# Kernel tuning notes

Hardware: AMD Instinct MI355X
Metric: run time of the kernel (lower is better)

## Reference

```python
import jax, jax.numpy as jnp
import numpy as np

B = 8          # batch size (static)
GRID = 1024    # spatial grid H = W
PER = 25000    # active sites per batch item
N = B * PER

_OFFSETS = [(dx, dy) for dx in (-1, 0, 1) for dy in (-1, 0, 1)]  # 3x3 kernel


def _build_sparse_inputs():
    """Sample unique active 2D coords per batch item and build the 3x3
    submanifold neighbor map: nbr[i, k] = index of neighbor site at kernel
    offset k, or -1 if that coordinate is inactive."""
    rng = np.random.default_rng(0)
    bs, xs, ys = [], [], []
    for b in range(B):
        flat = rng.choice(GRID * GRID, size=PER, replace=False)
        bs.append(np.full(PER, b, np.int64))
        xs.append((flat // GRID).astype(np.int64))
        ys.append((flat % GRID).astype(np.int64))
    bb = np.concatenate(bs); xx = np.concatenate(xs); yy = np.concatenate(ys)
    # hash lookup table: (b, x, y) -> site index
    lut = np.full(B * GRID * GRID, -1, np.int64)
    lut[bb * GRID * GRID + xx * GRID + yy] = np.arange(N, dtype=np.int64)
    nbr = np.full((N, 9), -1, np.int64)
    for k, (dx, dy) in enumerate(_OFFSETS):
        nx, ny = xx + dx, yy + dy
        ok = (nx >= 0) & (nx < GRID) & (ny >= 0) & (ny < GRID)
        key = bb * GRID * GRID + np.clip(nx, 0, GRID - 1) * GRID + np.clip(ny, 0, GRID - 1)
        nbr[:, k] = np.where(ok, lut[key], -1)
    return bb, nbr


def setup_inputs() -> dict:
    key = jax.random.key(0)
    k1, k2, k3 = jax.random.split(key, 3)
    batch_np, nbr_np = _build_sparse_inputs()
    feats = jax.random.normal(k1, (N, 3), dtype=jnp.float32)
    # He (kaiming normal, relu): std = sqrt(2 / fan_in), fan_in = 9 * Cin
    W1 = jax.random.normal(k2, (9, 3, 256), dtype=jnp.float32) * np.sqrt(2.0 / (9 * 3))
    W2 = jax.random.normal(k3, (9, 256, 256), dtype=jnp.float32) * np.sqrt(2.0 / (9 * 256))
    return {
        "feats": feats,
        "W1": W1,
        "W2": W2,
        "nbr": jnp.asarray(nbr_np),
        "batch_ids": jnp.asarray(batch_np),
    }


def _subm_conv(feat, W, nbr):
    """Submanifold 3x3 conv: out[i] = sum_k feat[nbr[i,k]] @ W[k] over valid
    neighbors. feat: [N, Cin], W: [9, Cin, Cout], nbr: [N, 9] -> [N, Cout]."""
    out = jnp.zeros((feat.shape[0], W.shape[2]), dtype=feat.dtype)
    for k in range(9):  # fixed small kernel loop
        idx = nbr[:, k]
        valid = (idx >= 0).astype(feat.dtype)[:, None]
        g = feat[jnp.maximum(idx, 0)] * valid  # masked gather [N, Cin]
        out = out + g @ W[k]
    return out


def reference(feats, W1, W2, nbr, batch_ids):
    h = jax.nn.relu(_subm_conv(feats, W1, nbr))   # [N, 256]
    h = jax.nn.relu(_subm_conv(h, W2, nbr))       # [N, 256]
    # global average pool per batch item -> [B, 256]
    sums = jax.ops.segment_sum(h, batch_ids, num_segments=B)
    counts = jax.ops.segment_sum(jnp.ones((h.shape[0],), h.dtype), batch_ids, num_segments=B)
    return sums / counts[:, None]
```

## Files before the change

### kernel.cpp

```cpp
#include <hip/hip_runtime.h>
#include <hip/hip_bf16.h>

typedef __attribute__((ext_vector_type(8))) short bh8;
typedef __attribute__((ext_vector_type(4))) float f32x4;

#define NB 8
#define SLOTS 64
#define CAP 6144
#define CROWS 36864
#define CBLOCKS 256
#define FROWS 64

__device__ __forceinline__ void gld_lds16(const void* g, void* l) {
  __builtin_amdgcn_global_load_lds(
      (const __attribute__((address_space(1))) void*)g,
      (__attribute__((address_space(3))) void*)l, 16, 0, 0);
}

__device__ __forceinline__ unsigned short f2bu(float f) {
  union { __hip_bfloat16 h; unsigned short u; } cv;
  cv.h = __float2bfloat16(f);
  return cv.u;
}
__device__ __forceinline__ float bu2f(unsigned short u) {
  return __uint_as_float(((unsigned)u) << 16);
}

__global__ void w1t_kernel(const float* __restrict__ W1, short* __restrict__ w1bt) {
  const int n = threadIdx.x;
#pragma unroll
  for (int kk = 0; kk < 32; ++kk)
    w1bt[n * 32 + kk] = (kk < 27) ? (short)f2bu(W1[kk * 256 + n]) : (short)0;
}

__device__ __forceinline__ float3 ldf3(const float* __restrict__ f,
                                       const int* s_nbr, int idx) {
  int s = s_nbr[idx];
  long long sc = (s < 0) ? 0 : s;
  float3 r;
  r.x = f[3 * sc]; r.y = f[3 * sc + 1]; r.z = f[3 * sc + 2];
  if (s < 0) { r.x = 0.f; r.y = 0.f; r.z = 0.f; }
  return r;
}

__global__ __launch_bounds__(256, 2) void conv1_mfma_kernel(
    const float* __restrict__ feats, const short* __restrict__ w1bt,
    const int* __restrict__ nbr, __hip_bfloat16* __restrict__ h1b, int N) {
  __shared__ int s_nbr[64 * 9];
  const int tid = threadIdx.x;
  const int base = blockIdx.x * 64;

  for (int t = tid; t < 64 * 9; t += 256) s_nbr[t] = nbr[base * 9 + t];
  __syncthreads();

  const int wave = tid >> 6, lane = tid & 63;
  const int q = lane >> 4, m16 = lane & 15;
  const int rbase = (wave * 16 + m16) * 9;

  bh8 a;
  if (q == 0) {
    float3 t0 = ldf3(feats, s_nbr, rbase + 0);
    float3 t1 = ldf3(feats, s_nbr, rbase + 1);
    float3 t2 = ldf3(feats, s_nbr, rbase + 2);
    a[0] = (short)f2bu(t0.x); a[1] = (short)f2bu(t0.y); a[2] = (short)f2bu(t0.z);
    a[3] = (short)f2bu(t1.x); a[4] = (short)f2bu(t1.y); a[5] = (short)f2bu(t1.z);
    a[6] = (short)f2bu(t2.x); a[7] = (short)f2bu(t2.y);
  } else if (q == 1) {
    float3 t2 = ldf3(feats, s_nbr, rbase + 2);
    float3 t3 = ldf3(feats, s_nbr, rbase + 3);
    float3 t4 = ldf3(feats, s_nbr, rbase + 4);
    float3 t5 = ldf3(feats, s_nbr, rbase + 5);
    a[0] = (short)f2bu(t2.z);
    a[1] = (short)f2bu(t3.x); a[2] = (short)f2bu(t3.y); a[3] = (short)f2bu(t3.z);
    a[4] = (short)f2bu(t4.x); a[5] = (short)f2bu(t4.y); a[6] = (short)f2bu(t4.z);
    a[7] = (short)f2bu(t5.x);
  } else if (q == 2) {
    float3 t5 = ldf3(feats, s_nbr, rbase + 5);
    float3 t6 = ldf3(feats, s_nbr, rbase + 6);
    float3 t7 = ldf3(feats, s_nbr, rbase + 7);
    a[0] = (short)f2bu(t5.y); a[1] = (short)f2bu(t5.z);
    a[2] = (short)f2bu(t6.x); a[3] = (short)f2bu(t6.y); a[4] = (short)f2bu(t6.z);
    a[5] = (short)f2bu(t7.x); a[6] = (short)f2bu(t7.y); a[7] = (short)f2bu(t7.z);
  } else {
    float3 t8 = ldf3(feats, s_nbr, rbase + 8);
    a[0] = (short)f2bu(t8.x); a[1] = (short)f2bu(t8.y); a[2] = (short)f2bu(t8.z);
    a[3] = 0; a[4] = 0; a[5] = 0; a[6] = 0; a[7] = 0;
  }

  f32x4 acc[16];
#pragma unroll
  for (int nj = 0; nj < 16; ++nj) {
    bh8 b = *(const bh8*)(w1bt + (nj * 16 + m16) * 32 + q * 8);
    acc[nj] = __builtin_amdgcn_mfma_f32_16x16x32_bf16(a, b, (f32x4)0.f, 0, 0, 0);
  }

  const int growb = base + wave * 16 + q * 4;
#pragma unroll
  for (int rr = 0; rr < 4; ++rr) {
    __hip_bfloat16* rowp = h1b + (long long)(growb + rr) * 256 + m16;
#pragma unroll
    for (int nj = 0; nj < 16; ++nj)
      rowp[nj * 16] = __float2bfloat16(fmaxf(acc[nj][rr], 0.f));
  }
}

__global__ __launch_bounds__(256) void w2t_kernel(
    const float* __restrict__ W2, __hip_bfloat16* __restrict__ w2bt) {
  __shared__ float tile[16][256];
  int k = blockIdx.x >> 4, t = blockIdx.x & 15;
  int tid = threadIdx.x;
#pragma unroll
  for (int r = 0; r < 16; ++r) tile[r][tid] = W2[k * 65536 + (t * 16 + r) * 256 + tid];
  __syncthreads();
#pragma unroll
  for (int r = 0; r < 16; ++r)
    w2bt[k * 65536 + tid * 256 + t * 16 + r] = __float2bfloat16(tile[r][tid]);
}

__global__ __launch_bounds__(256) void build_pairs_kernel(
    const int* __restrict__ nbr, const int* __restrict__ bid,
    int* __restrict__ nOff, int* __restrict__ cnt, float* __restrict__ bcnt,
    int* __restrict__ cidmap, int* __restrict__ crow,
    int* __restrict__ psrc, int* __restrict__ pcnt_cid,
    int* __restrict__ pairlist, int N) {
  __shared__ int l_cnt[10];
  __shared__ int l_base[10];
  __shared__ int l_bcnt[NB];
  const int tid = threadIdx.x;
  if (tid < 10) l_cnt[tid] = 0;
  if (tid < NB) l_bcnt[tid] = 0;
  __syncthreads();

  const int i = blockIdx.x * 256 + tid;
  const bool active = (i < N);
  int s[9];
  int kpos[9];
  int loc_cid = -1;
  if (active) {
#pragma unroll
    for (int k = 0; k < 9; ++k) s[k] = nbr[i * 9 + k];
    bool any = false;
#pragma unroll
    for (int k = 0; k < 9; ++k)
      if (k != 4 && s[k] >= 0) any = true;
    if (any) {
      loc_cid = atomicAdd(&l_cnt[9], 1);
#pragma unroll
      for (int k = 0; k < 9; ++k) {
        kpos[k] = -1;
        if (k != 4 && s[k] >= 0) kpos[k] = atomicAdd(&l_cnt[k], 1);
      }
    }
    atomicAdd(&l_bcnt[bid[i]], 1);
  }
  __syncthreads();

  if (tid < 9) l_base[tid] = (l_cnt[tid] > 0) ? atomicAdd(&cnt[tid], l_cnt[tid]) : 0;
  else if (tid == 9) l_base[9] = (l_cnt[9] > 0) ? atomicAdd(nOff, l_cnt[9]) : 0;
  if (tid >= 32 && tid < 32 + NB && l_bcnt[tid - 32] > 0)
    atomicAdd(&bcnt[tid - 32], (float)l_bcnt[tid - 32]);
  __syncthreads();

  if (active) {
    int cid = -1;
    if (loc_cid >= 0) {
      cid = l_base[9] + loc_cid;
      if (cid >= CROWS) cid = -1;
    }
    cidmap[i] = cid;
    if (cid >= 0) {
      crow[cid] = i;
#pragma unroll
      for (int k = 0; k < 9; ++k) {
        if (k == 4 || kpos[k] < 0 || s[k] < 0) continue;
        int pos = l_base[k] + kpos[k];
        if (pos < CAP) {
          psrc[k * CAP + pos] = s[k];
          int slot = atomicAdd(&pcnt_cid[cid], 1);
          if (slot < 8) pairlist[cid * 8 + slot] = k * CAP + pos;
        }
      }
    }
  }
}

__global__ __launch_bounds__(256, 2) void ctap_kernel(
    const __hip_bfloat16* __restrict__ h1, const __hip_bfloat16* __restrict__ w2bt,
    const int* __restrict__ nOffp, const int* __restrict__ crow,
    unsigned short* __restrict__ h2cb) {
  int nc = *nOffp;
  if (nc > CROWS) nc = CROWS;
  const int base = blockIdx.x * 64;
  if (base >= nc) return;

  __shared__ int s_src[64];
  const int tid = threadIdx.x;
  if (tid < 64) {
    int m = base + tid;
    s_src[tid] = (m < nc) ? crow[m] : 0;
  }

  const int wave = tid >> 6, lane = tid & 63, q = lane >> 4, m16 = lane & 15;
  const short* h1s = (const short*)h1;
  const short* wts = (const short*)w2bt + 4 * 65536;

  bh8 breg[4][8];
#pragma unroll
  for (int nj = 0; nj < 4; ++nj)
#pragma unroll
    for (int ko = 0; ko < 8; ++ko)
      breg[nj][ko] = *(const bh8*)(wts + (wave * 64 + nj * 16 + m16) * 256 + ko * 32 + q * 8);
  __syncthreads();

  bh8 aA[8];
  {
    const short* ap = h1s + (long long)s_src[m16] * 256 + q * 8;
#pragma unroll
    for (int ko = 0; ko < 8; ++ko) aA[ko] = *(const bh8*)(ap + ko * 32);
  }

#pragma unroll
  for (int t = 0; t < 4; ++t) {
    bh8 aN[8];
    if (t < 3) {
      const short* ap = h1s + (long long)s_src[(t + 1) * 16 + m16] * 256 + q * 8;
#pragma unroll
      for (int ko = 0; ko < 8; ++ko) aN[ko] = *(const bh8*)(ap + ko * 32);
    }
    f32x4 acc[4];
#pragma unroll
    for (int ko = 0; ko < 8; ++ko)
#pragma unroll
      for (int nj = 0; nj < 4; ++nj)
        acc[nj] = __builtin_amdgcn_mfma_f32_16x16x32_bf16(
            aA[ko], breg[nj][ko], (ko == 0) ? (f32x4)0.f : acc[nj], 0, 0, 0);
#pragma unroll
    for (int r = 0; r < 4; ++r) {
      int m = base + t * 16 + q * 4 + r;
      if (m >= nc) continue;
#pragma unroll
      for (int nj = 0; nj < 4; ++nj)
        h2cb[(long long)m * 256 + wave * 64 + nj * 16 + m16] = f2bu(acc[nj][r]);
    }
#pragma unroll
    for (int ko = 0; ko < 8; ++ko) aA[ko] = aN[ko];
    if (base + (t + 1) * 16 >= nc) break;
  }
}

__global__ __launch_bounds__(256, 2) void off_gemm_kernel(
    const __hip_bfloat16* __restrict__ h1, const __hip_bfloat16* __restrict__ w2bt,
    const int* __restrict__ cnt, const int* __restrict__ psrc,
    unsigned short* __restrict__ pout) {
  const int bpk = CAP / 64;
  int koff = blockIdx.x / bpk;
  int grp = blockIdx.x - koff * bpk;
  int k = koff + (koff >= 4 ? 1 : 0);
  int cntk = cnt[k];
  const int base = grp * 64;
  if (base >= cntk) return;

  __shared__ int s_src[64];
  const int tid = threadIdx.x;
  if (tid < 64) {
    int m = base + tid;
    s_src[tid] = (m < cntk) ? psrc[k * CAP + m] : 0;
  }

  const int wave = tid >> 6, lane = tid & 63, q = lane >> 4, m16 = lane & 15;
  const short* h1s = (const short*)h1;
  const short* wts = (const short*)w2bt + k * 65536;

  bh8 breg[4][8];
#pragma unroll
  for (int nj = 0; nj < 4; ++nj)
#pragma unroll
    for (int ko = 0; ko < 8; ++ko)
      breg[nj][ko] = *(const bh8*)(wts + (wave * 64 + nj * 16 + m16) * 256 + ko * 32 + q * 8);
  __syncthreads();

  bh8 aA[8];
  {
    const short* ap = h1s + (long long)s_src[m16] * 256 + q * 8;
#pragma unroll
    for (int ko = 0; ko < 8; ++ko) aA[ko] = *(const bh8*)(ap + ko * 32);
  }

#pragma unroll
  for (int t = 0; t < 4; ++t) {
    bh8 aN[8];
    if (t < 3) {
      const short* ap = h1s + (long long)s_src[(t + 1) * 16 + m16] * 256 + q * 8;
#pragma unroll
      for (int ko = 0; ko < 8; ++ko) aN[ko] = *(const bh8*)(ap + ko * 32);
    }
    f32x4 acc[4];
#pragma unroll
    for (int ko = 0; ko < 8; ++ko)
#pragma unroll
      for (int nj = 0; nj < 4; ++nj)
        acc[nj] = __builtin_amdgcn_mfma_f32_16x16x32_bf16(
            aA[ko], breg[nj][ko], (ko == 0) ? (f32x4)0.f : acc[nj], 0, 0, 0);
#pragma unroll
    for (int r = 0; r < 4; ++r) {
      int m = base + t * 16 + q * 4 + r;
      if (m >= cntk) continue;
      const long long rowb = (long long)(k * CAP + m) * 256;
#pragma unroll
      for (int nj = 0; nj < 4; ++nj)
        pout[rowb + wave * 64 + nj * 16 + m16] = f2bu(acc[nj][r]);
    }
#pragma unroll
    for (int ko = 0; ko < 8; ++ko) aA[ko] = aN[ko];
    if (base + (t + 1) * 16 >= cntk) break;
  }
}

__global__ __launch_bounds__(512, 2) void center_gemm_kernel(
    const __hip_bfloat16* __restrict__ h1, const __hip_bfloat16* __restrict__ w2bt,
    const int* __restrict__ cidmap, const int* __restrict__ bid,
    float* __restrict__ psums, int N) {
  __shared__ __align__(16) short Abuf[2][64 * 256];

  const int tid = threadIdx.x;
  const int wave = tid >> 6, lane = tid & 63;
  const int q = lane >> 4, m16 = lane & 15;
  const int wc = wave << 5;
  const int slot = blockIdx.x & (SLOTS - 1);

  const short* h1s = (const short*)h1;
  const short* wts = (const short*)w2bt + 4 * 65536;

  bh8 breg[2][8];
#pragma unroll
  for (int nj = 0; nj < 2; ++nj)
#pragma unroll
    for (int ko = 0; ko < 8; ++ko)
      breg[nj][ko] = *(const bh8*)(wts + (wc + nj * 16 + m16) * 256 + ko * 32 + q * 8);

  const int nchunk = (N + 63) >> 6;
  const int span = (nchunk + CBLOCKS - 1) / CBLOCKS;
  const int c0 = blockIdx.x * span;
  if (c0 >= nchunk) return;
  int c1 = c0 + span;
  if (c1 > nchunk) c1 = nchunk;

  const int lrow = lane >> 5;
  const int jch  = lane & 31;

#define STAGE_CHUNK(cc, b)                                                     \
  {                                                                            \
    _Pragma("unroll") for (int t = 0; t < 4; ++t) {                            \
      int lr = (wave << 3) + (t << 1) + lrow;                                  \
      int g = ((cc) << 6) + lr;                                                \
      if (g >= N) g = N - 1;                                                   \
      int js = jch ^ (lr & 31);                                                \
      const short* src = h1s + (long long)g * 256 + (js << 3);                 \
      short* dst = &Abuf[b][((wave << 3) + (t << 1)) << 8];                    \
      gld_lds16((const void*)src, (void*)dst);                                 \
    }                                                                          \
  }

#define FLUSH_SACC()                                                           \
  if (cur_b0 >= 0) {                                                           \
    _Pragma("unroll") for (int lb = 0; lb < 2; ++lb) {                         \
      _Pragma("unroll") for (int nj = 0; nj < 2; ++nj) {                       \
        float v = sacc[lb][nj];                                                \
        v += __shfl_xor(v, 16, 64);                                            \
        v += __shfl_xor(v, 32, 64);                                            \
        if (q == 0 && v != 0.f) {                                              \
          int b = cur_b0 + lb;                                                 \
          if (b < NB)                                                          \
            atomicAdd(&psums[(slot * NB + b) * 256 + wc + nj * 16 + m16], v);  \
        }                                                                      \
      }                                                                        \
    }                                                                          \
  }

  STAGE_CHUNK(c0, 0);
  int cur = 0;
  int cur_b0 = -1;
  float sacc[2][2];
#pragma unroll
  for (int lb = 0; lb < 2; ++lb)
#pragma unroll
    for (int nj = 0; nj < 2; ++nj) sacc[lb][nj] = 0.f;

  for (int c = c0; c < c1; ++c) {
    __syncthreads();

    int4 bid4[4], cid4[4];
#pragma unroll
    for (int mi = 0; mi < 4; ++mi) {
      const int rb = (c << 6) + mi * 16 + q * 4;
      bid4[mi] = *(const int4*)(&bid[rb]);
      cid4[mi] = *(const int4*)(&cidmap[rb]);
    }
    const int b0 = bid[c << 6];

    if (c + 1 < c1) STAGE_CHUNK(c + 1, cur ^ 1);

    const short* Ab = &Abuf[cur][0];
    const short* abase[4];
    int xr[4];
#pragma unroll
    for (int mi = 0; mi < 4; ++mi) {
      int R = mi * 16 + m16;
      xr[mi] = R & 31;
      abase[mi] = Ab + (R << 8);
    }

    f32x4 acc[4][2];
#pragma unroll
    for (int ko = 0; ko < 8; ++ko) {
      bh8 a[4];
#pragma unroll
      for (int mi = 0; mi < 4; ++mi)
        a[mi] = *(const bh8*)(abase[mi] + (((ko * 4 + q) ^ xr[mi]) << 3));
#pragma unroll
      for (int mi = 0; mi < 4; ++mi)
#pragma unroll
        for (int nj = 0; nj < 2; ++nj)
          acc[mi][nj] = __builtin_amdgcn_mfma_f32_16x16x32_bf16(
              a[mi], breg[nj][ko], (ko == 0) ? (f32x4)0.f : acc[mi][nj], 0, 0, 0);
    }

    if (b0 != cur_b0) {
      FLUSH_SACC();
#pragma unroll
      for (int lb = 0; lb < 2; ++lb)
#pragma unroll
        for (int nj = 0; nj < 2; ++nj) sacc[lb][nj] = 0.f;
      cur_b0 = b0;
    }
#pragma unroll
    for (int mi = 0; mi < 4; ++mi) {
      const int bb[4] = {bid4[mi].x, bid4[mi].y, bid4[mi].z, bid4[mi].w};
      const int cc4[4] = {cid4[mi].x, cid4[mi].y, cid4[mi].z, cid4[mi].w};
      const int rb = (c << 6) + mi * 16 + q * 4;
#pragma unroll
      for (int rr = 0; rr < 4; ++rr) {
        if (rb + rr >= N) continue;
        if (cc4[rr] >= 0) continue;
        const int lb = (bb[rr] != b0) ? 1 : 0;
#pragma unroll
        for (int nj = 0; nj < 2; ++nj)
          sacc[lb][nj] += fmaxf(acc[mi][nj][rr], 0.f);
      }
    }

    cur ^= 1;
  }
  FLUSH_SACC();
#undef STAGE_CHUNK
#undef FLUSH_SACC
}

__global__ __launch_bounds__(256) void fixup_kernel(
    const unsigned short* __restrict__ h2cb, const unsigned short* __restrict__ pout,
    const int* __restrict__ pairlist, const int* __restrict__ pcnt_cid,
    const int* __restrict__ crow, const int* __restrict__ bid,
    const int* __restrict__ nOffp, float* __restrict__ psums) {
  __shared__ float lsum[NB * 256];
  __shared__ int s_b[FROWS], s_np[FROWS], s_pl[FROWS * 8];
  int nc = *nOffp;
  if (nc > CROWS) nc = CROWS;
  const int t0 = blockIdx.x * FROWS;
  if (t0 >= nc) return;
  const int tid = threadIdx.x;

  if (tid < FROWS) {
    int m = t0 + tid;
    bool v = (m < nc);
    s_b[tid] = v ? bid[crow[m]] : -1;
    int np = v ? pcnt_cid[m] : 0;
    s_np[tid] = (np > 8) ? 8 : np;
  }
  for (int i = tid; i < FROWS * 8; i += 256) {
    int m = t0 + (i >> 3);
    s_pl[i] = (m < nc) ? pairlist[m * 8 + (i & 7)] : 0;
  }
#pragma unroll
  for (int b = 0; b < NB; ++b) lsum[b * 256 + tid] = 0.f;
  __syncthreads();

  const int g = tid >> 6;
  const int cg = tid & 63;
  const ushort4* h2v = (const ushort4*)h2cb;
  const ushort4* pov = (const ushort4*)pout;

  float4 s0 = {0.f, 0.f, 0.f, 0.f}, s1 = {0.f, 0.f, 0.f, 0.f};
  const int r0 = g * 16;
  const int b0 = s_b[r0];
  int b1 = -1;
  for (int r = r0; r < r0 + 16; ++r) {
    const int b = s_b[r];
    if (b < 0) break;
    ushort4 u = h2v[(long long)(t0 + r) * 64 + cg];
    float4 x = {bu2f(u.x), bu2f(u.y), bu2f(u.z), bu2f(u.w)};
    const int np = s_np[r];
    for (int j = 0; j < np; ++j) {
      ushort4 p = pov[(long long)s_pl[r * 8 + j] * 64 + cg];
      x.x += bu2f(p.x); x.y += bu2f(p.y); x.z += bu2f(p.z); x.w += bu2f(p.w);
    }
    x.x = fmaxf(x.x, 0.f); x.y = fmaxf(x.y, 0.f);
    x.z = fmaxf(x.z, 0.f); x.w = fmaxf(x.w, 0.f);
    if (b == b0) {
      s0.x += x.x; s0.y += x.y; s0.z += x.z; s0.w += x.w;
    } else {
      b1 = b;
      s1.x += x.x; s1.y += x.y; s1.z += x.z; s1.w += x.w;
    }
  }
  if (b0 >= 0) {
    float* p0 = &lsum[b0 * 256 + cg * 4];
    atomicAdd(p0 + 0, s0.x); atomicAdd(p0 + 1, s0.y);
    atomicAdd(p0 + 2, s0.z); atomicAdd(p0 + 3, s0.w);
  }
  if (b1 >= 0 && b1 < NB) {
    float* p1 = &lsum[b1 * 256 + cg * 4];
    atomicAdd(p1 + 0, s1.x); atomicAdd(p1 + 1, s1.y);
    atomicAdd(p1 + 2, s1.z); atomicAdd(p1 + 3, s1.w);
  }
  __syncthreads();

  const int slot = blockIdx.x & (SLOTS - 1);
#pragma unroll
  for (int b = 0; b < NB; ++b) {
    float v = lsum[b * 256 + tid];
    if (v != 0.f) atomicAdd(&psums[(slot * NB + b) * 256 + tid], v);
  }
}

__global__ void finalize_kernel(const float* __restrict__ psums,
                                const float* __restrict__ bcnt,
                                float* __restrict__ out) {
  int b = blockIdx.x, c = threadIdx.x;
  float s = 0.f;
  for (int t = 0; t < SLOTS; ++t) s += psums[(t * NB + b) * 256 + c];
  out[b * 256 + c] = s / bcnt[b];
}

extern "C" void kernel_launch(void* const* d_in, const int* in_sizes, int n_in,
                              void* d_out, int out_size, void* d_ws, size_t ws_size,
                              hipStream_t stream) {
  const float* feats = (const float*)d_in[0];
  const float* W1    = (const float*)d_in[1];
  const float* W2    = (const float*)d_in[2];
  const int*   nbr   = (const int*)d_in[3];
  const int*   bid   = (const int*)d_in[4];
  float* out = (float*)d_out;
  const int N = in_sizes[0] / 3;

  char* ws = (char*)d_ws;
  size_t o = 0;
  float* psums = (float*)(ws + o); o += (size_t)SLOTS * NB * 256 * 4;
  float* bcnt  = (float*)(ws + o); o += NB * 4;
  int*   nOff  = (int*)(ws + o);   o += 4;
  int*   cnt   = (int*)(ws + o);   o += 9 * 4;
  o = (o + 255) & ~(size_t)255;
  int* pcnt_cid = (int*)(ws + o); o += (size_t)CROWS * 4;
  size_t zero1 = o;
  int* psrc = (int*)(ws + o); o += (size_t)9 * CAP * 4;
  int* pairlist = (int*)(ws + o); o += (size_t)CROWS * 8 * 4;
  int* cidmap = (int*)(ws + o); o += (size_t)N * 4;
  int* crow = (int*)(ws + o); o += (size_t)CROWS * 4;
  o = (o + 255) & ~(size_t)255;
  unsigned short* h2cb = (unsigned short*)(ws + o); o += (size_t)CROWS * 256 * 2;
  unsigned short* pout = (unsigned short*)(ws + o); o += (size_t)9 * CAP * 256 * 2;
  __hip_bfloat16* w2bt = (__hip_bfloat16*)(ws + o); o += (size_t)9 * 65536 * 2;
  short* w1bt = (short*)(ws + o); o += (size_t)256 * 32 * 2;
  __hip_bfloat16* h1b  = (__hip_bfloat16*)(ws + o); o += (size_t)N * 256 * 2;

  hipMemsetAsync(d_ws, 0, zero1, stream);

  w1t_kernel<<<1, 256, 0, stream>>>(W1, w1bt);
  conv1_mfma_kernel<<<(N + 63) / 64, 256, 0, stream>>>(feats, w1bt, nbr, h1b, N);
  w2t_kernel<<<9 * 16, 256, 0, stream>>>(W2, w2bt);
  build_pairs_kernel<<<(N + 255) / 256, 256, 0, stream>>>(
      nbr, bid, nOff, cnt, bcnt, cidmap, crow, psrc, pcnt_cid, pairlist, N);
  ctap_kernel<<<CROWS / 64, 256, 0, stream>>>(h1b, w2bt, nOff, crow, h2cb);
  off_gemm_kernel<<<8 * (CAP / 64), 256, 0, stream>>>(h1b, w2bt, cnt, psrc, pout);
  center_gemm_kernel<<<CBLOCKS, 512, 0, stream>>>(h1b, w2bt, cidmap, bid, psums, N);
  fixup_kernel<<<(CROWS + FROWS - 1) / FROWS, 256, 0, stream>>>(
      h2cb, pout, pairlist, pcnt_cid, crow, bid, nOff, psums);
  finalize_kernel<<<NB, 256, 0, stream>>>(psums, bcnt, out);
}
```

Measured before the change: 270.0 us.

## Fuse center-tap output into center GEMM, stage conv1 stores via LDS, double center blocks

The separate ctap kernel recomputed the center-tap GEMM for rows that have active neighbors. Those rows are now written to h2cb directly from the center GEMM's accumulators, which removes one kernel and a second pass over their h1 rows. The conv1 output is transposed through a padded LDS tile so each thread writes 16-byte coalesced stores instead of scattered 2-byte stores. The center GEMM grid is doubled to 512 blocks. The LDS tile adds about 33KB of shared memory per conv1 block, which may reduce occupancy.

Result: no change. 271.6 us (+0.6%).

```diff
diff --git a/kernel.cpp b/kernel.cpp
--- a/kernel.cpp
+++ b/kernel.cpp
@@ -8,8 +8,9 @@
 #define SLOTS 64
 #define CAP 6144
 #define CROWS 36864
-#define CBLOCKS 256
+#define CBLOCKS 512
 #define FROWS 64
+#define TSTRIDE 264
 
 __device__ __forceinline__ void gld_lds16(const void* g, void* l) {
   __builtin_amdgcn_global_load_lds(
@@ -47,6 +48,7 @@
     const float* __restrict__ feats, const short* __restrict__ w1bt,
     const int* __restrict__ nbr, __hip_bfloat16* __restrict__ h1b, int N) {
   __shared__ int s_nbr[64 * 9];
+  __shared__ unsigned short tile[64 * TSTRIDE];
   const int tid = threadIdx.x;
   const int base = blockIdx.x * 64;
 
@@ -94,13 +96,20 @@
     acc[nj] = __builtin_amdgcn_mfma_f32_16x16x32_bf16(a, b, (f32x4)0.f, 0, 0, 0);
   }
 
-  const int growb = base + wave * 16 + q * 4;
-#pragma unroll
-  for (int rr = 0; rr < 4; ++rr) {
-    __hip_bfloat16* rowp = h1b + (long long)(growb + rr) * 256 + m16;
-#pragma unroll
-    for (int nj = 0; nj < 16; ++nj)
-      rowp[nj * 16] = __float2bfloat16(fmaxf(acc[nj][rr], 0.f));
+#pragma unroll
+  for (int nj = 0; nj < 16; ++nj)
+#pragma unroll
+    for (int rr = 0; rr < 4; ++rr)
+      tile[(wave * 16 + q * 4 + rr) * TSTRIDE + nj * 16 + m16] =
+          f2bu(fmaxf(acc[nj][rr], 0.f));
+  __syncthreads();
+
+  {
+    const int row = tid >> 2, seg = tid & 3;
+    const int4* src = (const int4*)&tile[row * TSTRIDE + seg * 64];
+    int4* dst = (int4*)(h1b + (long long)(base + row) * 256 + seg * 64);
+#pragma unroll
+    for (int i = 0; i < 8; ++i) dst[i] = src[i];
   }
 }
 
@@ -184,70 +193,6 @@
   }
 }
 
-__global__ __launch_bounds__(256, 2) void ctap_kernel(
-    const __hip_bfloat16* __restrict__ h1, const __hip_bfloat16* __restrict__ w2bt,
-    const int* __restrict__ nOffp, const int* __restrict__ crow,
-    unsigned short* __restrict__ h2cb) {
-  int nc = *nOffp;
-  if (nc > CROWS) nc = CROWS;
-  const int base = blockIdx.x * 64;
-  if (base >= nc) return;
-
-  __shared__ int s_src[64];
-  const int tid = threadIdx.x;
-  if (tid < 64) {
-    int m = base + tid;
-    s_src[tid] = (m < nc) ? crow[m] : 0;
-  }
-
-  const int wave = tid >> 6, lane = tid & 63, q = lane >> 4, m16 = lane & 15;
-  const short* h1s = (const short*)h1;
-  const short* wts = (const short*)w2bt + 4 * 65536;
-
-  bh8 breg[4][8];
-#pragma unroll
-  for (int nj = 0; nj < 4; ++nj)
-#pragma unroll
-    for (int ko = 0; ko < 8; ++ko)
-      breg[nj][ko] = *(const bh8*)(wts + (wave * 64 + nj * 16 + m16) * 256 + ko * 32 + q * 8);
-  __syncthreads();
-
-  bh8 aA[8];
-  {
-    const short* ap = h1s + (long long)s_src[m16] * 256 + q * 8;
-#pragma unroll
-    for (int ko = 0; ko < 8; ++ko) aA[ko] = *(const bh8*)(ap + ko * 32);
-  }
-
-#pragma unroll
-  for (int t = 0; t < 4; ++t) {
-    bh8 aN[8];
-    if (t < 3) {
-      const short* ap = h1s + (long long)s_src[(t + 1) * 16 + m16] * 256 + q * 8;
-#pragma unroll
-      for (int ko = 0; ko < 8; ++ko) aN[ko] = *(const bh8*)(ap + ko * 32);
-    }
-    f32x4 acc[4];
-#pragma unroll
-    for (int ko = 0; ko < 8; ++ko)
-#pragma unroll
-      for (int nj = 0; nj < 4; ++nj)
-        acc[nj] = __builtin_amdgcn_mfma_f32_16x16x32_bf16(
-            aA[ko], breg[nj][ko], (ko == 0) ? (f32x4)0.f : acc[nj], 0, 0, 0);
-#pragma unroll
-    for (int r = 0; r < 4; ++r) {
-      int m = base + t * 16 + q * 4 + r;
-      if (m >= nc) continue;
-#pragma unroll
-      for (int nj = 0; nj < 4; ++nj)
-        h2cb[(long long)m * 256 + wave * 64 + nj * 16 + m16] = f2bu(acc[nj][r]);
-    }
-#pragma unroll
-    for (int ko = 0; ko < 8; ++ko) aA[ko] = aN[ko];
-    if (base + (t + 1) * 16 >= nc) break;
-  }
-}
-
 __global__ __launch_bounds__(256, 2) void off_gemm_kernel(
     const __hip_bfloat16* __restrict__ h1, const __hip_bfloat16* __restrict__ w2bt,
     const int* __restrict__ cnt, const int* __restrict__ psrc,
@@ -319,7 +264,7 @@
 __global__ __launch_bounds__(512, 2) void center_gemm_kernel(
     const __hip_bfloat16* __restrict__ h1, const __hip_bfloat16* __restrict__ w2bt,
     const int* __restrict__ cidmap, const int* __restrict__ bid,
-    float* __restrict__ psums, int N) {
+    float* __restrict__ psums, unsigned short* __restrict__ h2cb, int N) {
   __shared__ __align__(16) short Abuf[2][64 * 256];
 
   const int tid = threadIdx.x;
@@ -441,7 +386,12 @@
 #pragma unroll
       for (int rr = 0; rr < 4; ++rr) {
         if (rb + rr >= N) continue;
-        if (cc4[rr] >= 0) continue;
+        if (cc4[rr] >= 0) {
+          unsigned short* hp = h2cb + (long long)cc4[rr] * 256 + wc + m16;
+          hp[0] = f2bu(acc[mi][0][rr]);
+          hp[16] = f2bu(acc[mi][1][rr]);
+          continue;
+        }
         const int lb = (bb[rr] != b0) ? 1 : 0;
 #pragma unroll
         for (int nj = 0; nj < 2; ++nj)
@@ -579,9 +529,9 @@
   w2t_kernel<<<9 * 16, 256, 0, stream>>>(W2, w2bt);
   build_pairs_kernel<<<(N + 255) / 256, 256, 0, stream>>>(
       nbr, bid, nOff, cnt, bcnt, cidmap, crow, psrc, pcnt_cid, pairlist, N);
-  ctap_kernel<<<CROWS / 64, 256, 0, stream>>>(h1b, w2bt, nOff, crow, h2cb);
   off_gemm_kernel<<<8 * (CAP / 64), 256, 0, stream>>>(h1b, w2bt, cnt, psrc, pout);
-  center_gemm_kernel<<<CBLOCKS, 512, 0, stream>>>(h1b, w2bt, cidmap, bid, psums, N);
+  center_gemm_kernel<<<CBLOCKS, 512, 0, stream>>>(h1b, w2bt, cidmap, bid, psums,
+                                                  h2cb, N);
   fixup_kernel<<<(CROWS + FROWS - 1) / FROWS, 256, 0, stream>>>(
       h2cb, pout, pairlist, pcnt_cid, crow, bid, nOff, psums);
   finalize_kernel<<<NB, 256, 0, stream>>>(psums, bcnt, out);
```
